# Kernel tuning notes

Measured on AMD Instinct MI355X. Metric: run time of the kernel, lower is better.

The kernel has to match this reference:

```python
import jax, jax.numpy as jnp
import numpy as np
from jax import lax
from jax.scipy.special import logsumexp

B, T, N, D = 64, 4096, 32, 64  # subjects, seq_len, states, obs_dim
LOG_2PI = float(np.log(2.0 * np.pi))


def setup_inputs() -> dict:
    key = jax.random.key(0)
    k1, k2, k3, k4, k5 = jax.random.split(key, 5)
    X = jax.random.normal(k1, (B, T, D), dtype=jnp.float32)
    # unnormalized logits; original inits to uniform 1/N, we perturb for a non-trivial test
    transition_matrix = jnp.ones((N, N), jnp.float32) / N + 0.05 * jax.random.normal(k2, (N, N), dtype=jnp.float32)
    state_priors = jnp.ones((N,), jnp.float32) / N + 0.05 * jax.random.normal(k3, (N,), dtype=jnp.float32)
    # per-state diagonal-Gaussian emission params
    mus = jax.random.normal(k4, (N, D), dtype=jnp.float32)
    log_vars = 0.1 * jax.random.normal(k5, (N, D), dtype=jnp.float32)
    return {"X": X, "transition_matrix": transition_matrix, "state_priors": state_priors,
            "mus": mus, "log_vars": log_vars}


def _emission_logprobs(X, mus, log_vars):
    # X: (B,T,D); mus, log_vars: (N,D) -> log N(x; mu_n, diag(var_n)): (B,T,N)
    inv_var = jnp.exp(-log_vars)                                   # (N,D)
    # expand quadratic form to avoid the (B,T,N,D) intermediate
    quad = (jnp.einsum('btd,nd->btn', X * X, inv_var)
            - 2.0 * jnp.einsum('btd,nd->btn', X, mus * inv_var)
            + jnp.sum(mus * mus * inv_var, axis=-1))               # (B,T,N)
    return -0.5 * (quad + jnp.sum(log_vars, axis=-1) + D * LOG_2PI)


def reference(X, transition_matrix, state_priors, mus, log_vars):
    log_A = jax.nn.log_softmax(transition_matrix, axis=1)   # F.log_softmax picks dim=1 for 2D
    log_pi = jax.nn.log_softmax(state_priors, axis=0)
    logB = _emission_logprobs(X, mus, log_vars)             # (B,T,N)

    alpha0 = log_pi + logB[:, 0, :]                         # (B,N)

    def step(prev, logb_t):
        # log_alpha[t] = emission[t] + logsumexp_i(log_alpha[t-1,i] + log_A[i,j])
        a = logb_t + logsumexp(prev[:, :, None] + log_A[None, :, :], axis=1)
        return a, a

    _, alphas = lax.scan(step, alpha0, jnp.moveaxis(logB[:, 1:, :], 1, 0))  # (T-1,B,N)
    log_alpha = jnp.concatenate([alpha0[:, None, :], jnp.moveaxis(alphas, 0, 1)], axis=1)  # (B,T,N)
    log_prob = logsumexp(log_alpha, axis=2)                 # (B,T)
    return log_prob
```

## Files before the change

kernel.cpp:

```cpp
#include <hip/hip_runtime.h>
#include <hip/hip_bf16.h>
#include <stdint.h>

#define BB 64
#define TT 4096
#define NS 32
#define DD 64
#define CH 256
#define CL 16
#define WU 8
#define NSTEPS (WU + CL)
#define LOG2PI 1.8378770664093453f
#define LN2F 0.6931471805599453f
#define FLT_MIN_NORM 1.175494350822288e-38f

typedef float f32x16 __attribute__((ext_vector_type(16)));
typedef __bf16 bf16x8 __attribute__((ext_vector_type(8)));

__device__ __forceinline__ uint32_t cvt_pk_bf16(float lo, float hi) {
  uint32_t d;
  asm("v_cvt_pk_bf16_f32 %0, %1, %2" : "=v"(d) : "v"(lo), "v"(hi));
  return d;
}

__device__ __forceinline__ float dpp_max64(float v) {
  float r = v; int x;
  x = __builtin_amdgcn_update_dpp(__float_as_int(r), __float_as_int(r), 0x111, 0xF, 0xF, false); r = fmaxf(r, __int_as_float(x));
  x = __builtin_amdgcn_update_dpp(__float_as_int(r), __float_as_int(r), 0x112, 0xF, 0xF, false); r = fmaxf(r, __int_as_float(x));
  x = __builtin_amdgcn_update_dpp(__float_as_int(r), __float_as_int(r), 0x114, 0xF, 0xF, false); r = fmaxf(r, __int_as_float(x));
  x = __builtin_amdgcn_update_dpp(__float_as_int(r), __float_as_int(r), 0x118, 0xF, 0xF, false); r = fmaxf(r, __int_as_float(x));
  x = __builtin_amdgcn_update_dpp(__float_as_int(r), __float_as_int(r), 0x142, 0xF, 0xF, false); r = fmaxf(r, __int_as_float(x));
  x = __builtin_amdgcn_update_dpp(__float_as_int(r), __float_as_int(r), 0x143, 0xF, 0xF, false); r = fmaxf(r, __int_as_float(x));
  return r;
}


__global__ __launch_bounds__(1024) void k_pre(
    const float* __restrict__ tm, const float* __restrict__ sp,
    const float* __restrict__ mus, const float* __restrict__ lv,
    float* __restrict__ pivec, uint32_t* __restrict__ Wp,
    float* __restrict__ bias, uint32_t* __restrict__ Af)
{
  __shared__ float As[32][32];
  const int tid = threadIdx.x;
  const int row = tid >> 5;
  const int col = tid & 31;

  {
    float v = tm[row * 32 + col];
    float m = v;
    #pragma unroll
    for (int mask = 16; mask; mask >>= 1) m = fmaxf(m, __shfl_xor(m, mask));
    float e = __expf(v - m);
    float s = e;
    #pragma unroll
    for (int mask = 16; mask; mask >>= 1) s += __shfl_xor(s, mask);
    As[row][col] = e / s;
  }

  if (tid < 32) {
    float v = sp[tid];
    float m = v;
    #pragma unroll
    for (int mask = 16; mask; mask >>= 1) m = fmaxf(m, __shfl_xor(m, mask));
    float e = __expf(v - m);
    float s = e;
    #pragma unroll
    for (int mask = 16; mask; mask >>= 1) s += __shfl_xor(s, mask);
    pivec[tid] = e / s;
  }

  #pragma unroll
  for (int hh = 0; hh < 2; ++hh) {
    int d = col + (hh << 5);
    float iv = __expf(-lv[row * 64 + d]);
    uint32_t w = cvt_pk_bf16(-0.5f * iv, mus[row * 64 + d] * iv);
    int kk = d >> 3, h2 = (d >> 2) & 1, j = d & 3;
    Wp[(((row << 1) + h2) * 8 + kk) * 4 + j] = w;
  }

  {
    float s2 = 0.f, slv = 0.f;
    #pragma unroll
    for (int h = 0; h < 2; ++h) {
      int d = col + h * 32;
      float m_ = mus[row * 64 + d];
      float l_ = lv[row * 64 + d];
      s2 = fmaf(m_ * m_, __expf(-l_), s2);
      slv += l_;
    }
    #pragma unroll
    for (int mask = 16; mask; mask >>= 1) {
      s2  += __shfl_xor(s2, mask);
      slv += __shfl_xor(slv, mask);
    }
    if (col == 0) bias[row] = -0.5f * (s2 + slv + (float)DD * LOG2PI);
  }

  __syncthreads();

  if (tid < 512) {
    int l = tid >> 3, s = tid & 7;
    int m = s >> 2, p = s & 3;
    int j = l & 31, hh = l >> 5;
    int r0 = 2 * p, r1 = r0 + 1;
    int s0 = (r0 & 3) + 8 * ((r0 >> 2) & 1) + 4 * hh + 16 * m;
    int s1 = (r1 & 3) + 8 * ((r1 >> 2) & 1) + 4 * hh + 16 * m;
    Af[(l << 3) + (m << 2) + p] = cvt_pk_bf16(As[s0][j], As[s1][j]);
  }
}

__global__ __launch_bounds__(256) void k_fused(
    const float* __restrict__ Xg,
    const uint32_t* __restrict__ Wp,
    const float* __restrict__ bias,
    const uint32_t* __restrict__ Af,
    const float* __restrict__ pivec,
    float* __restrict__ out,
    float* __restrict__ Mc)
{
  __shared__ uint32_t blinL[544 * 16];
  __shared__ float KcL[32];
  const int tid = threadIdx.x;
  const int l   = tid & 63;
  const int wv  = tid >> 6;
  const int g   = blockIdx.x;
  const int b   = g >> 3;
  const int cb  = g & 7;
  const int t0  = cb << 9;
  const int n   = l & 31;
  const int h   = l >> 5;

  uint4 wf[8];
  const uint4* wp4 = (const uint4*)(Wp + ((n << 1) + h) * 32);
  #pragma unroll
  for (int kk = 0; kk < 8; ++kk) wf[kk] = wp4[kk];
  const float bn = bias[n];

  for (int wi = wv; wi < 17; wi += 4) {
    if (cb == 0 && wi == 0) continue;
    const int wbase = t0 - 32 + (wi << 5);
    const float* xr = Xg + (size_t)(b * TT + wbase + n) * DD + (h << 2);

    f32x16 acc;
    #pragma unroll
    for (int r = 0; r < 16; ++r) acc[r] = 0.0f;

    #pragma unroll
    for (int kk = 0; kk < 8; ++kk) {
      float4 x4 = *(const float4*)(xr + (kk << 3));
      uint4 au;
      au.x = cvt_pk_bf16(x4.x * x4.x, x4.x);
      au.y = cvt_pk_bf16(x4.y * x4.y, x4.y);
      au.z = cvt_pk_bf16(x4.z * x4.z, x4.z);
      au.w = cvt_pk_bf16(x4.w * x4.w, x4.w);
      bf16x8 af = __builtin_bit_cast(bf16x8, au);
      bf16x8 bf = __builtin_bit_cast(bf16x8, wf[kk]);
      acc = __builtin_amdgcn_mfma_f32_32x32x16_bf16(af, bf, acc, 0, 0, 0);
    }

    float lb[16];
    float m0 = -1e30f, m1 = -1e30f;
    #pragma unroll
    for (int r = 0; r < 16; ++r) {
      lb[r] = acc[r] + bn;
      if (r < 8) m0 = fmaxf(m0, lb[r]); else m1 = fmaxf(m1, lb[r]);
    }
    m0 = dpp_max64(m0);
    m1 = dpp_max64(m1);
    const float Km0 = __int_as_float(__builtin_amdgcn_readlane(__float_as_int(m0), 63));
    const float Km1 = __int_as_float(__builtin_amdgcn_readlane(__float_as_int(m1), 63));
    if (wi >= 1 && l == 0) {
      KcL[((wi - 1) << 1)]     = Km0;
      KcL[((wi - 1) << 1) + 1] = Km1;
    }

    const int rb = wi << 5;
    #pragma unroll
    for (int r = 0; r < 16; ++r) {
      float e = __expf(lb[r] - ((r < 8) ? Km0 : Km1));
      int nb = __builtin_amdgcn_update_dpp(0, __float_as_int(e), 0xB1, 0xF, 0xF, true);
      uint32_t pk = cvt_pk_bf16(e, __int_as_float(nb));
      const int ldsrow = rb + (r & 3) + ((r >> 2) << 3) + (h << 2);
      if ((l & 1) == 0)
        blinL[ldsrow * 16 + ((n >> 1) ^ (((ldsrow >> 4) & 7) << 1))] = pk;
    }
  }
  __syncthreads();
  if (wv != 0) return;

  const int col = n;
  const int c   = (cb << 5) + col;
  const bool isC0 = (cb == 0) && (col == 0);

  const uint4 af0u = *(const uint4*)(Af + (l << 3));
  const uint4 af1u = *(const uint4*)(Af + (l << 3) + 4);
  const bf16x8 af0 = __builtin_bit_cast(bf16x8, af0u);
  const bf16x8 af1 = __builtin_bit_cast(bf16x8, af1u);

  const float KcH = KcL[col];
  const int outbase = b * TT + (c << 4);

  f32x16 zv;
  #pragma unroll
  for (int r = 0; r < 16; ++r) zv[r] = 0.0f;

  float v[16];
  #pragma unroll
  for (int r = 0; r < 16; ++r) v[r] = 1.0f;
  float S = 0.0f, sPrev = 1.0f;

  #pragma unroll
  for (int q = 0; q < NSTEPS; ++q) {
    float sP = fmaxf(sPrev, FLT_MIN_NORM);
    int e = ((__float_as_int(sP) >> 23) & 0xFF) - 126;
    float rf = __int_as_float((127 - e) << 23);
    if (q >= WU) {
      float outv = __log2f(sP) * LN2F + S;
      if (q == WU) { if (h == 0) Mc[(b << 8) + c] = outv; }
      else         { if (h == 0) out[outbase + q - WU - 1] = outv; }
      S += KcH + (float)e * LN2F;
    } else {
      S += (float)e * LN2F;
    }

    int ldsrow = 24 + (col << 4) + q;
    if (cb == 0 && ldsrow < 32) ldsrow = 32;
    const int swz = ((ldsrow >> 4) & 7) << 1;
    const uint32_t* p = blinL + ldsrow * 16;
    const int h2 = h << 1;
    uint2 u0 = *(const uint2*)(p + (h2 ^ swz));
    uint2 u1 = *(const uint2*)(p + ((h2 + 4) ^ swz));
    uint2 u2 = *(const uint2*)(p + ((h2 + 8) ^ swz));
    uint2 u3 = *(const uint2*)(p + ((h2 + 12) ^ swz));
    uint32_t CUR[8];
    CUR[0] = u0.x; CUR[1] = u0.y; CUR[2] = u1.x; CUR[3] = u1.y;
    CUR[4] = u2.x; CUR[5] = u2.y; CUR[6] = u3.x; CUR[7] = u3.y;

    float vr[16];
    #pragma unroll
    for (int r = 0; r < 16; ++r) vr[r] = v[r] * rf;
    uint32_t p2[8];
    #pragma unroll
    for (int i = 0; i < 8; ++i) p2[i] = cvt_pk_bf16(vr[2*i], vr[2*i+1]);
    uint4 b0u; b0u.x = p2[0]; b0u.y = p2[1]; b0u.z = p2[2]; b0u.w = p2[3];
    uint4 b1u; b1u.x = p2[4]; b1u.y = p2[5]; b1u.z = p2[6]; b1u.w = p2[7];
    f32x16 acc = __builtin_amdgcn_mfma_f32_32x32x16_bf16(af0, __builtin_bit_cast(bf16x8, b0u), zv, 0, 0, 0);
    acc = __builtin_amdgcn_mfma_f32_32x32x16_bf16(af1, __builtin_bit_cast(bf16x8, b1u), acc, 0, 0, 0);

    #pragma unroll
    for (int i = 0; i < 8; ++i) {
      float blo = __int_as_float(CUR[i] << 16);
      float bhi = __int_as_float(CUR[i] & 0xFFFF0000u);
      float d0 = acc[2*i], d1 = acc[2*i+1];
      if (q == WU) { if (isC0) { d0 = vr[2*i]; d1 = vr[2*i+1]; } }
      v[2*i]   = d0 * blo;
      v[2*i+1] = d1 * bhi;
    }
    if (q == WU - 1) {
      if (isC0) {
        #pragma unroll
        for (int r = 0; r < 16; ++r)
          v[r] = pivec[(r & 3) + 8 * ((r >> 2) & 1) + (h << 2) + ((r >> 3) << 4)];
        S = 0.0f;
      }
    }
    float s8[8];
    #pragma unroll
    for (int i = 0; i < 8; ++i) s8[i] = v[2*i] + v[2*i+1];
    float s4a = s8[0] + s8[1], s4b = s8[2] + s8[3];
    float s4c = s8[4] + s8[5], s4d = s8[6] + s8[7];
    float s = (s4a + s4b) + (s4c + s4d);
    s += __shfl_xor(s, 32);
    sPrev = s;
  }

  {
    float sP = fmaxf(sPrev, FLT_MIN_NORM);
    if (h == 0) out[outbase + CL - 1] = __log2f(sP) * LN2F + S;
  }
}

__global__ void k_stitch(const float* __restrict__ out, const float* __restrict__ Mcc,
                         float* __restrict__ Delta)
{
  __shared__ float wsum[4];
  const int b  = blockIdx.x;
  const int c  = threadIdx.x;
  const int wv = c >> 6, ln = c & 63;
  float term = 0.0f;
  if (c > 0) term = out[b * TT + (c << 4) - 1] - Mcc[(b << 8) + c];
  for (int off = 1; off < 64; off <<= 1) {
    float up = __shfl_up(term, off);
    if (ln >= off) term += up;
  }
  if (ln == 63) wsum[wv] = term;
  __syncthreads();
  float add = 0.0f;
  for (int i = 0; i < wv; ++i) add += wsum[i];
  Delta[(b << 8) + c] = term + add;
}

__global__ void k_add(float* __restrict__ out, const float* __restrict__ Delta)
{
  const int i = blockIdx.x * 256 + threadIdx.x;
  const int b = i >> 12;
  const int t = i & 4095;
  out[i] += Delta[(b << 8) + (t >> 4)];
}

extern "C" void kernel_launch(void* const* d_in, const int* in_sizes, int n_in,
                              void* d_out, int out_size, void* d_ws, size_t ws_size,
                              hipStream_t stream) {
  const float* X   = (const float*)d_in[0];
  const float* tm  = (const float*)d_in[1];
  const float* sp  = (const float*)d_in[2];
  const float* mus = (const float*)d_in[3];
  const float* lv  = (const float*)d_in[4];
  float* out = (float*)d_out;

  char* ws = (char*)d_ws;
  size_t off = 0;
  float* Mcc   = (float*)(ws + off); off += (size_t)BB * CH * 4;
  float* Delta = (float*)(ws + off); off += (size_t)BB * CH * 4;
  float* pivec = (float*)(ws + off); off += 256;
  uint32_t* Wp = (uint32_t*)(ws + off); off += (size_t)2048 * 4;
  float* bias  = (float*)(ws + off); off += 256;
  uint32_t* Af = (uint32_t*)(ws + off); off += (size_t)512 * 4;

  k_pre<<<dim3(1), dim3(1024), 0, stream>>>(tm, sp, mus, lv, pivec, Wp, bias, Af);
  k_fused<<<dim3(512), dim3(256), 0, stream>>>(X, Wp, bias, Af, pivec, out, Mcc);
  k_stitch<<<dim3(BB), dim3(256), 0, stream>>>(out, Mcc, Delta);
  k_add<<<dim3((BB * TT) / 256), dim3(256), 0, stream>>>(out, Delta);
}
```

Baseline: 34.07 us.

## Fold parameter preprocessing into main kernel and merge stitch with add

Removes the single-block k_pre launch. Each k_fused block now computes the transition softmax, the prior softmax, the packed emission weights, the bias and the MFMA A-fragments itself, using shared memory. k_stitch and k_add become one k_post kernel that keeps the prefix-sum offsets in LDS and applies them directly to the output. This cuts four launches to two and drops the workspace round-trips, at the cost of repeating the small parameter preprocessing in every block, including a 64-iteration per-lane bias loop with exp.

After: 38.49 us. 1.13x slower.

```diff
diff --git a/kernel.cpp b/kernel.cpp
--- a/kernel.cpp
+++ b/kernel.cpp
@@ -35,92 +35,19 @@
 }
 
 
-__global__ __launch_bounds__(1024) void k_pre(
-    const float* __restrict__ tm, const float* __restrict__ sp,
-    const float* __restrict__ mus, const float* __restrict__ lv,
-    float* __restrict__ pivec, uint32_t* __restrict__ Wp,
-    float* __restrict__ bias, uint32_t* __restrict__ Af)
-{
-  __shared__ float As[32][32];
-  const int tid = threadIdx.x;
-  const int row = tid >> 5;
-  const int col = tid & 31;
-
-  {
-    float v = tm[row * 32 + col];
-    float m = v;
-    #pragma unroll
-    for (int mask = 16; mask; mask >>= 1) m = fmaxf(m, __shfl_xor(m, mask));
-    float e = __expf(v - m);
-    float s = e;
-    #pragma unroll
-    for (int mask = 16; mask; mask >>= 1) s += __shfl_xor(s, mask);
-    As[row][col] = e / s;
-  }
-
-  if (tid < 32) {
-    float v = sp[tid];
-    float m = v;
-    #pragma unroll
-    for (int mask = 16; mask; mask >>= 1) m = fmaxf(m, __shfl_xor(m, mask));
-    float e = __expf(v - m);
-    float s = e;
-    #pragma unroll
-    for (int mask = 16; mask; mask >>= 1) s += __shfl_xor(s, mask);
-    pivec[tid] = e / s;
-  }
-
-  #pragma unroll
-  for (int hh = 0; hh < 2; ++hh) {
-    int d = col + (hh << 5);
-    float iv = __expf(-lv[row * 64 + d]);
-    uint32_t w = cvt_pk_bf16(-0.5f * iv, mus[row * 64 + d] * iv);
-    int kk = d >> 3, h2 = (d >> 2) & 1, j = d & 3;
-    Wp[(((row << 1) + h2) * 8 + kk) * 4 + j] = w;
-  }
-
-  {
-    float s2 = 0.f, slv = 0.f;
-    #pragma unroll
-    for (int h = 0; h < 2; ++h) {
-      int d = col + h * 32;
-      float m_ = mus[row * 64 + d];
-      float l_ = lv[row * 64 + d];
-      s2 = fmaf(m_ * m_, __expf(-l_), s2);
-      slv += l_;
-    }
-    #pragma unroll
-    for (int mask = 16; mask; mask >>= 1) {
-      s2  += __shfl_xor(s2, mask);
-      slv += __shfl_xor(slv, mask);
-    }
-    if (col == 0) bias[row] = -0.5f * (s2 + slv + (float)DD * LOG2PI);
-  }
-
-  __syncthreads();
-
-  if (tid < 512) {
-    int l = tid >> 3, s = tid & 7;
-    int m = s >> 2, p = s & 3;
-    int j = l & 31, hh = l >> 5;
-    int r0 = 2 * p, r1 = r0 + 1;
-    int s0 = (r0 & 3) + 8 * ((r0 >> 2) & 1) + 4 * hh + 16 * m;
-    int s1 = (r1 & 3) + 8 * ((r1 >> 2) & 1) + 4 * hh + 16 * m;
-    Af[(l << 3) + (m << 2) + p] = cvt_pk_bf16(As[s0][j], As[s1][j]);
-  }
-}
-
 __global__ __launch_bounds__(256) void k_fused(
     const float* __restrict__ Xg,
-    const uint32_t* __restrict__ Wp,
-    const float* __restrict__ bias,
-    const uint32_t* __restrict__ Af,
-    const float* __restrict__ pivec,
+    const float* __restrict__ tm,
+    const float* __restrict__ sp,
+    const float* __restrict__ mus,
+    const float* __restrict__ lv,
     float* __restrict__ out,
     float* __restrict__ Mc)
 {
   __shared__ uint32_t blinL[544 * 16];
+  __shared__ float As[32][32];
   __shared__ float KcL[32];
+  __shared__ float pivL[32];
   const int tid = threadIdx.x;
   const int l   = tid & 63;
   const int wv  = tid >> 6;
@@ -131,11 +58,54 @@
   const int n   = l & 31;
   const int h   = l >> 5;
 
+  #pragma unroll
+  for (int rr = 0; rr < 4; ++rr) {
+    const int row = (wv << 3) + (rr << 1) + h;
+    float vv = tm[row * 32 + n];
+    float m = vv;
+    #pragma unroll
+    for (int mask = 16; mask; mask >>= 1) m = fmaxf(m, __shfl_xor(m, mask));
+    float e = __expf(vv - m);
+    float s = e;
+    #pragma unroll
+    for (int mask = 16; mask; mask >>= 1) s += __shfl_xor(s, mask);
+    As[row][n] = e / s;
+  }
+  if (tid < 32) {
+    float vv = sp[tid];
+    float m = vv;
+    #pragma unroll
+    for (int mask = 16; mask; mask >>= 1) m = fmaxf(m, __shfl_xor(m, mask));
+    float e = __expf(vv - m);
+    float s = e;
+    #pragma unroll
+    for (int mask = 16; mask; mask >>= 1) s += __shfl_xor(s, mask);
+    pivL[tid] = e / s;
+  }
   uint4 wf[8];
-  const uint4* wp4 = (const uint4*)(Wp + ((n << 1) + h) * 32);
-  #pragma unroll
-  for (int kk = 0; kk < 8; ++kk) wf[kk] = wp4[kk];
-  const float bn = bias[n];
+  #pragma unroll
+  for (int kk = 0; kk < 8; ++kk) {
+    uint32_t wj[4];
+    #pragma unroll
+    for (int j = 0; j < 4; ++j) {
+      const int d = (kk << 3) + (h << 2) + j;
+      float iv = __expf(-lv[n * 64 + d]);
+      wj[j] = cvt_pk_bf16(-0.5f * iv, mus[n * 64 + d] * iv);
+    }
+    wf[kk].x = wj[0]; wf[kk].y = wj[1]; wf[kk].z = wj[2]; wf[kk].w = wj[3];
+  }
+  float bn;
+  {
+    float s2 = 0.f, slv = 0.f;
+    #pragma unroll
+    for (int d = 0; d < 64; ++d) {
+      float m_ = mus[n * 64 + d];
+      float l_ = lv[n * 64 + d];
+      s2 = fmaf(m_ * m_, __expf(-l_), s2);
+      slv += l_;
+    }
+    bn = -0.5f * (s2 + slv + (float)DD * LOG2PI);
+  }
 
   for (int wi = wv; wi < 17; wi += 4) {
     if (cb == 0 && wi == 0) continue;
@@ -193,8 +163,19 @@
   const int c   = (cb << 5) + col;
   const bool isC0 = (cb == 0) && (col == 0);
 
-  const uint4 af0u = *(const uint4*)(Af + (l << 3));
-  const uint4 af1u = *(const uint4*)(Af + (l << 3) + 4);
+  uint32_t afw[8];
+  #pragma unroll
+  for (int m = 0; m < 2; ++m) {
+    #pragma unroll
+    for (int p = 0; p < 4; ++p) {
+      const int r0 = 2 * p, r1 = r0 + 1;
+      const int s0 = (r0 & 3) + 8 * ((r0 >> 2) & 1) + (h << 2) + (m << 4);
+      const int s1 = (r1 & 3) + 8 * ((r1 >> 2) & 1) + (h << 2) + (m << 4);
+      afw[(m << 2) + p] = cvt_pk_bf16(As[s0][n], As[s1][n]);
+    }
+  }
+  uint4 af0u; af0u.x = afw[0]; af0u.y = afw[1]; af0u.z = afw[2]; af0u.w = afw[3];
+  uint4 af1u; af1u.x = afw[4]; af1u.y = afw[5]; af1u.z = afw[6]; af1u.w = afw[7];
   const bf16x8 af0 = __builtin_bit_cast(bf16x8, af0u);
   const bf16x8 af1 = __builtin_bit_cast(bf16x8, af1u);
 
@@ -261,7 +242,7 @@
       if (isC0) {
         #pragma unroll
         for (int r = 0; r < 16; ++r)
-          v[r] = pivec[(r & 3) + 8 * ((r >> 2) & 1) + (h << 2) + ((r >> 3) << 4)];
+          v[r] = pivL[(r & 3) + 8 * ((r >> 2) & 1) + (h << 2) + ((r >> 3) << 4)];
         S = 0.0f;
       }
     }
@@ -281,9 +262,10 @@
   }
 }
 
-__global__ void k_stitch(const float* __restrict__ out, const float* __restrict__ Mcc,
-                         float* __restrict__ Delta)
+__global__ __launch_bounds__(256) void k_post(
+    float* __restrict__ out, const float* __restrict__ Mcc)
 {
+  __shared__ float DeltaL[256];
   __shared__ float wsum[4];
   const int b  = blockIdx.x;
   const int c  = threadIdx.x;
@@ -298,15 +280,11 @@
   __syncthreads();
   float add = 0.0f;
   for (int i = 0; i < wv; ++i) add += wsum[i];
-  Delta[(b << 8) + c] = term + add;
-}
-
-__global__ void k_add(float* __restrict__ out, const float* __restrict__ Delta)
-{
-  const int i = blockIdx.x * 256 + threadIdx.x;
-  const int b = i >> 12;
-  const int t = i & 4095;
-  out[i] += Delta[(b << 8) + (t >> 4)];
+  DeltaL[c] = term + add;
+  __syncthreads();
+  #pragma unroll
+  for (int t = c; t < TT; t += 256)
+    out[b * TT + t] += DeltaL[t >> 4];
 }
 
 extern "C" void kernel_launch(void* const* d_in, const int* in_sizes, int n_in,
@@ -319,17 +297,8 @@
   const float* lv  = (const float*)d_in[4];
   float* out = (float*)d_out;
 
-  char* ws = (char*)d_ws;
-  size_t off = 0;
-  float* Mcc   = (float*)(ws + off); off += (size_t)BB * CH * 4;
-  float* Delta = (float*)(ws + off); off += (size_t)BB * CH * 4;
-  float* pivec = (float*)(ws + off); off += 256;
-  uint32_t* Wp = (uint32_t*)(ws + off); off += (size_t)2048 * 4;
-  float* bias  = (float*)(ws + off); off += 256;
-  uint32_t* Af = (uint32_t*)(ws + off); off += (size_t)512 * 4;
-
-  k_pre<<<dim3(1), dim3(1024), 0, stream>>>(tm, sp, mus, lv, pivec, Wp, bias, Af);
-  k_fused<<<dim3(512), dim3(256), 0, stream>>>(X, Wp, bias, Af, pivec, out, Mcc);
-  k_stitch<<<dim3(BB), dim3(256), 0, stream>>>(out, Mcc, Delta);
-  k_add<<<dim3((BB * TT) / 256), dim3(256), 0, stream>>>(out, Delta);
-}
+  float* Mcc = (float*)d_ws;
+
+  k_fused<<<dim3(512), dim3(256), 0, stream>>>(X, tm, sp, mus, lv, out, Mcc);
+  k_post<<<dim3(BB), dim3(256), 0, stream>>>(out, Mcc);
+}
```
